# Optimization experiments

Hardware: AMD Instinct MI355X
Metric: run time of the kernel (lower is better)

## Reference

```python
import jax, jax.numpy as jnp
import numpy as np

L, H, DH = 4, 8, 64            # num_layers, num_heads, hidden_dim (= dim_per_head)
HD = H * DH                    # 512 = per-layer q/k/v width
R, BLOCK, NREG, NW = 3, 128, 8, 8   # n_hashes, block_size, num_regions, num_w_per_dist
CDIM, LAT = 2, 3               # coords_dim, latent_dim
SCALE = 1.0 / float(np.sqrt(DH))


def layer_norm(x, g, b):
    m = x.mean(-1, keepdims=True)
    v = ((x - m) ** 2).mean(-1, keepdims=True)
    return (x - m) * jax.lax.rsqrt(v + 1e-5) * g + b


def hept_attention(q, k, v, coords, batch, w_head, hash_proj):
    # HEPT: E2LSH hash + region/batch bucketing -> sort -> blockwise attention
    # with RPE distance bias, combined over hash rounds by logsumexp weights.
    N = q.shape[0]
    nb = N // BLOCK
    qh = q.reshape(N, H, DH)
    kh = k.reshape(N, H, DH)
    vh = v.reshape(N, H, DH)
    c0 = coords[:, 0]
    region = jnp.clip(((c0 - c0.min()) / (c0.max() - c0.min() + 1e-6) * NREG).astype(jnp.int32), 0, NREG - 1)
    c_rpe = coords[:, 1:]                       # [N, CDIM-1] dims used for RPE distances
    bf = batch.astype(jnp.float32)
    outs, lses = [], []
    for r in range(R):
        hv = coords @ hash_proj[r]              # [N] LSH projection
        hn = (hv - hv.min()) / (hv.max() - hv.min() + 1e-6)
        skey = (bf * NREG + region.astype(jnp.float32)) * 2.0 + hn  # batch-major, region, hash
        idx = jnp.argsort(skey)
        inv = jnp.argsort(idx)
        qs = qh[idx].reshape(nb, BLOCK, H, DH)
        ks = kh[idx].reshape(nb, BLOCK, H, DH)
        vs = vh[idx].reshape(nb, BLOCK, H, DH)
        cs = c_rpe[idx].reshape(nb, BLOCK, CDIM - 1)
        bs = batch[idx].reshape(nb, BLOCK)
        scores = jnp.einsum('bihd,bjhd->bhij', qs, ks) * SCALE     # [nb,H,B,B]
        d2 = (cs[:, :, None, :] - cs[:, None, :, :]) ** 2          # [nb,B,B,CDIM-1]
        scores = scores - jnp.einsum('hc,bijc->bhij', w_head, d2)  # RPE distance penalty
        scores = jnp.where((bs[:, :, None] == bs[:, None, :])[:, None], scores, -1e9)
        lse = jax.nn.logsumexp(scores, axis=-1)                    # [nb,H,B]
        p = jnp.exp(scores - lse[..., None])
        o = jnp.einsum('bhij,bjhd->bihd', p, vs).reshape(N, H, DH)
        outs.append(o[inv])
        lses.append(jnp.transpose(lse, (0, 2, 1)).reshape(N, H)[inv])
    wts = jax.nn.softmax(jnp.stack(lses), axis=0)[..., None]       # [R,N,H,1]
    return (wts * jnp.stack(outs)).sum(0).reshape(N, HD)


def _forward(x, coords, batch, enc_W1, enc_b1, enc_W2, enc_b2, ln1_g, ln1_b, wq, wk, wv,
             rpe_W, wo, ln2_g, ln2_b, ff_W1, ff_b1, ff_W2, ff_b2, W_cat,
             mlp_W1, mlp_b1, mlp_W2, mlp_b2, beta_W1, beta_b1, beta_W2, beta_b2,
             coord_W1, coord_b1, coord_W2, coord_b2, hash_proj):
    h0 = jax.nn.relu(x @ enc_W1 + enc_b1) @ enc_W2 + enc_b2
    feats = [h0]
    cur = h0
    for l in range(L):
        xn = layer_norm(cur, ln1_g[l], ln1_b[l])
        q = xn @ wq[l]
        k = xn @ wk[l]
        v = xn @ wv[l]
        # per-head positive RPE weights derived from w_rpe weight matrix
        w_head = jax.nn.softplus(rpe_W[l].reshape(CDIM - 1, NW, H, DH).mean(axis=(1, 3)).T)  # [H,CDIM-1]
        a = hept_attention(q, k, v, coords, batch, w_head, hash_proj) @ wo[l]
        cur = cur + a
        ffo = jax.nn.relu(layer_norm(cur, ln2_g[l], ln2_b[l]) @ ff_W1[l] + ff_b1[l]) @ ff_W2[l] + ff_b2[l]
        cur = cur + ffo
        feats.append(cur)
    enc2 = jnp.concatenate(feats, axis=-1) @ W_cat
    out = enc2 + (jax.nn.relu(enc2 @ mlp_W1 + mlp_b1) @ mlp_W2 + mlp_b2)
    eps = 1e-6
    beta = jnp.clip(jax.nn.sigmoid(jax.nn.relu(out @ beta_W1 + beta_b1) @ beta_W2 + beta_b2), eps, 1.0 - eps)
    hcoord = jax.nn.relu(out @ coord_W1 + coord_b1) @ coord_W2 + coord_b2
    return beta, hcoord


def setup_inputs() -> dict:
    key = jax.random.key(0)
    ks = jax.random.split(key, 40)
    N, IN_DIM = 32768, 16
    def w(i, shape, s=0.05):
        return jax.random.normal(ks[i], shape, jnp.float32) * s
    return dict(
        x=jax.random.normal(ks[0], (N, IN_DIM), jnp.float32),
        coords=jax.random.normal(ks[1], (N, CDIM), jnp.float32),
        batch=jnp.sort(jax.random.randint(ks[2], (N,), 0, 8)),
        enc_W1=w(3, (IN_DIM, DH)), enc_b1=jnp.zeros((DH,), jnp.float32),
        enc_W2=w(4, (DH, DH)), enc_b2=jnp.zeros((DH,), jnp.float32),
        ln1_g=jnp.ones((L, DH), jnp.float32), ln1_b=jnp.zeros((L, DH), jnp.float32),
        wq=w(5, (L, DH, HD)), wk=w(6, (L, DH, HD)), wv=w(7, (L, DH, HD)),
        rpe_W=w(8, (L, NW * (CDIM - 1), HD)),
        wo=w(9, (L, HD, DH)),
        ln2_g=jnp.ones((L, DH), jnp.float32), ln2_b=jnp.zeros((L, DH), jnp.float32),
        ff_W1=w(10, (L, DH, DH)), ff_b1=jnp.zeros((L, DH), jnp.float32),
        ff_W2=w(11, (L, DH, DH)), ff_b2=jnp.zeros((L, DH), jnp.float32),
        W_cat=w(12, (DH * (L + 1), DH // 2)),
        mlp_W1=w(13, (DH // 2, DH // 2)), mlp_b1=jnp.zeros((DH // 2,), jnp.float32),
        mlp_W2=w(14, (DH // 2, DH // 2)), mlp_b2=jnp.zeros((DH // 2,), jnp.float32),
        beta_W1=w(15, (DH // 2, DH // 4)), beta_b1=jnp.zeros((DH // 4,), jnp.float32),
        beta_W2=w(16, (DH // 4, 1)), beta_b2=jnp.zeros((1,), jnp.float32),
        coord_W1=w(17, (DH // 2, DH // 4)), coord_b1=jnp.zeros((DH // 4,), jnp.float32),
        coord_W2=w(18, (DH // 4, LAT)), coord_b2=jnp.zeros((LAT,), jnp.float32),
        hash_proj=jax.random.normal(ks[19], (R, CDIM), jnp.float32),
    )


def reference(x, coords, batch, enc_W1, enc_b1, enc_W2, enc_b2, ln1_g, ln1_b, wq, wk, wv,
              rpe_W, wo, ln2_g, ln2_b, ff_W1, ff_b1, ff_W2, ff_b2, W_cat,
              mlp_W1, mlp_b1, mlp_W2, mlp_b2, beta_W1, beta_b1, beta_W2, beta_b2,
              coord_W1, coord_b1, coord_W2, coord_b2, hash_proj):
    return _forward(x, coords, batch, enc_W1, enc_b1, enc_W2, enc_b2, ln1_g, ln1_b, wq, wk, wv,
                    rpe_W, wo, ln2_g, ln2_b, ff_W1, ff_b1, ff_W2, ff_b2, W_cat,
                    mlp_W1, mlp_b1, mlp_W2, mlp_b2, beta_W1, beta_b1, beta_W2, beta_b2,
                    coord_W1, coord_b1, coord_W2, coord_b2, hash_proj)
```

## Files before the change

### kernel.cpp

```cpp
#include <hip/hip_runtime.h>
#include <math.h>

#define DEV __device__ __forceinline__

constexpr int DHc = 64;
constexpr int HDc = 512;
constexpr int Hc  = 8;
constexpr int BLKc = 128;

typedef float f32x16 __attribute__((ext_vector_type(16)));
typedef short s16x8  __attribute__((ext_vector_type(8)));

union FragU { unsigned u[4]; s16x8 v; };

DEV unsigned fenc(float f){ unsigned u = __float_as_uint(f); return (u & 0x80000000u) ? ~u : (u | 0x80000000u); }
DEV float fdec(unsigned u){ unsigned b = (u & 0x80000000u) ? (u ^ 0x80000000u) : ~u; return __uint_as_float(b); }
DEV float hv_calc(float c0, float c1, float h0, float h1){
  return __fadd_rn(__fmul_rn(c0, h0), __fmul_rn(c1, h1));
}
DEV unsigned short f2bf(float f){
  unsigned u = __float_as_uint(f);
  return (unsigned short)((u + 0x7FFFu + ((u >> 16) & 1u)) >> 16);
}
DEV float bf2f(unsigned short s){ return __uint_as_float((unsigned)s << 16); }

DEV unsigned cvtpk(float lo, float hi){
  unsigned r;
  asm("v_cvt_pk_bf16_f32 %0, %1, %2" : "=v"(r) : "v"(lo), "v"(hi));
  return r;
}
DEV unsigned pack_bf2(float lo, float hi){
  return (unsigned)f2bf(lo) | ((unsigned)f2bf(hi) << 16);
}
DEV void pswap(unsigned &a, unsigned &b){
  asm volatile("v_permlane32_swap_b32 %0, %1" : "+v"(a), "+v"(b));
}

__global__ void minmax_init_kernel(unsigned* mm){
  int t = threadIdx.x;
  if (t < 4) mm[t] = 0xFFFFFFFFu;
  else if (t < 8) mm[t] = 0u;
}

__global__ __launch_bounds__(256) void minmax_reduce_kernel(const float* __restrict__ coords,
    const float* __restrict__ hp, unsigned* mm, int N)
{
  __shared__ float red[4][8];
  float h[6];
  #pragma unroll
  for (int i = 0; i < 6; ++i) h[i] = hp[i];
  float mn[4] = {3.0e38f, 3.0e38f, 3.0e38f, 3.0e38f};
  float mx[4] = {-3.0e38f, -3.0e38f, -3.0e38f, -3.0e38f};
  for (int i = blockIdx.x*blockDim.x + threadIdx.x; i < N; i += gridDim.x*blockDim.x){
    float2 c = *(const float2*)&coords[2*i];
    float v0 = c.x;
    float v1 = hv_calc(c.x, c.y, h[0], h[1]);
    float v2 = hv_calc(c.x, c.y, h[2], h[3]);
    float v3 = hv_calc(c.x, c.y, h[4], h[5]);
    mn[0] = fminf(mn[0], v0); mx[0] = fmaxf(mx[0], v0);
    mn[1] = fminf(mn[1], v1); mx[1] = fmaxf(mx[1], v1);
    mn[2] = fminf(mn[2], v2); mx[2] = fmaxf(mx[2], v2);
    mn[3] = fminf(mn[3], v3); mx[3] = fmaxf(mx[3], v3);
  }
  #pragma unroll
  for (int o = 1; o < 64; o <<= 1){
    #pragma unroll
    for (int s = 0; s < 4; ++s){
      mn[s] = fminf(mn[s], __shfl_xor(mn[s], o));
      mx[s] = fmaxf(mx[s], __shfl_xor(mx[s], o));
    }
  }
  int w = threadIdx.x >> 6;
  if ((threadIdx.x & 63) == 0){
    #pragma unroll
    for (int s = 0; s < 4; ++s){ red[w][s] = mn[s]; red[w][4+s] = mx[s]; }
  }
  __syncthreads();
  int t = threadIdx.x;
  if (t < 4){
    float v = fminf(fminf(red[0][t], red[1][t]), fminf(red[2][t], red[3][t]));
    atomicMin(&mm[t], fenc(v));
  } else if (t < 8){
    float v = fmaxf(fmaxf(red[0][t], red[1][t]), fmaxf(red[2][t], red[3][t]));
    atomicMax(&mm[t], fenc(v));
  }
}

__global__ void make_keys_kernel(const float* __restrict__ coords, const int* __restrict__ batch,
                                 const float* __restrict__ hp, const unsigned* __restrict__ mm,
                                 unsigned long long* __restrict__ keys, int N)
{
  int i = blockIdx.x*blockDim.x + threadIdx.x;
  if (i >= N) return;
  float c0 = coords[2*i], c1 = coords[2*i+1];
  float c0min = fdec(mm[0]), c0max = fdec(mm[4]);
  float rf = (c0 - c0min) / (c0max - c0min + 1e-6f) * 8.0f;
  int region = (int)rf;
  region = region < 0 ? 0 : (region > 7 ? 7 : region);
  float base2 = ((float)batch[i] * 8.0f + (float)region) * 2.0f;
  #pragma unroll
  for (int r = 0; r < 3; ++r){
    float hv = hv_calc(c0, c1, hp[2*r], hp[2*r+1]);
    float hn = (hv - fdec(mm[1+r])) / (fdec(mm[5+r]) - fdec(mm[1+r]) + 1e-6f);
    float skey = base2 + hn;
    keys[(size_t)r*N + i] = ((unsigned long long)__float_as_uint(skey) << 32) | (unsigned)i;
  }
}

__global__ __launch_bounds__(1024) void bitonic_local_full2k_kernel(unsigned long long* keys, int N)
{
  __shared__ unsigned long long sh[2048];
  unsigned long long* a = keys + (size_t)blockIdx.y * N;
  int base = blockIdx.x * 2048, t = threadIdx.x;
  sh[t] = a[base + t];
  sh[t + 1024] = a[base + t + 1024];
  __syncthreads();
  for (int k = 2; k <= 2048; k <<= 1){
    for (int j = k >> 1; j > 0; j >>= 1){
      int i = ((t & ~(j-1)) << 1) | (t & (j-1));
      bool dirup = (((base + i) & k) == 0);
      unsigned long long x = sh[i], y = sh[i+j];
      if ((x > y) == dirup){ sh[i] = y; sh[i+j] = x; }
      __syncthreads();
    }
  }
  a[base + t] = sh[t];
  a[base + t + 1024] = sh[t + 1024];
}

__global__ void bitonic_global_kernel(unsigned long long* keys, int N, int k, int j)
{
  unsigned long long* a = keys + (size_t)blockIdx.y * N;
  int i = blockIdx.x*blockDim.x + threadIdx.x;
  int l = i ^ j;
  if (l > i && l < N){
    unsigned long long x = a[i], y = a[l];
    bool dirup = ((i & k) == 0);
    if ((x > y) == dirup){ a[i] = y; a[l] = x; }
  }
}

__global__ __launch_bounds__(1024) void bitonic_local_merge2k_kernel(unsigned long long* keys, int N, int k)
{
  __shared__ unsigned long long sh[2048];
  unsigned long long* a = keys + (size_t)blockIdx.y * N;
  int base = blockIdx.x * 2048, t = threadIdx.x;
  sh[t] = a[base + t];
  sh[t + 1024] = a[base + t + 1024];
  __syncthreads();
  for (int j = 1024; j > 0; j >>= 1){
    int i = ((t & ~(j-1)) << 1) | (t & (j-1));
    bool dirup = (((base + i) & k) == 0);
    unsigned long long x = sh[i], y = sh[i+j];
    if ((x > y) == dirup){ sh[i] = y; sh[i+j] = x; }
    __syncthreads();
  }
  a[base + t] = sh[t];
  a[base + t + 1024] = sh[t + 1024];
}

__global__ void extract_idx_kernel(const unsigned long long* __restrict__ keys, int* __restrict__ idx, int total)
{
  int i = blockIdx.x*blockDim.x + threadIdx.x;
  if (i < total) idx[i] = (int)(keys[i] & 0xFFFFFFFFull);
}

__global__ void wconv_kernel(const float* __restrict__ wq, const float* __restrict__ wk,
                             const float* __restrict__ wv, const float* __restrict__ wo,
                             unsigned short* __restrict__ wqkvT, unsigned short* __restrict__ woT)
{
  int tid = blockIdx.x*blockDim.x + threadIdx.x;
  const int NQ = 4*3*512*64;
  if (tid < NQ){
    int kk = tid & 63;
    int rest = tid >> 6;
    int n = rest & 511;
    int rest2 = rest >> 9;
    int z = rest2 % 3, l = rest2 / 3;
    const float* W = (z==0) ? wq : (z==1) ? wk : wv;
    wqkvT[tid] = f2bf(W[((size_t)l*64 + kk)*512 + n]);
  } else if (tid < NQ + 4*64*512){
    int e = tid - NQ;
    int kk = e & 511;
    int rest = e >> 9;
    int n = rest & 63;
    int l = rest >> 6;
    woT[e] = f2bf(wo[((size_t)l*512 + kk)*64 + n]);
  }
}

__global__ __launch_bounds__(256) void mqk_kernel(const float* __restrict__ wq,
    const float* __restrict__ wk, unsigned short* __restrict__ mqk)
{
  __shared__ float qs[64][64];
  __shared__ float ks_[64][64];
  int blk = blockIdx.x;
  int l = blk >> 3, h = blk & 7;
  int t = threadIdx.x;
  for (int f = t; f < 4096; f += 256){
    int i = f >> 6, d = f & 63;
    qs[i][d]  = wq[((size_t)l*64 + i)*512 + h*64 + d];
    ks_[i][d] = wk[((size_t)l*64 + i)*512 + h*64 + d];
  }
  __syncthreads();
  int j = t >> 2, i0 = (t & 3) * 16;
  unsigned short* outp = mqk + (size_t)blk*4096 + j*64;
  #pragma unroll
  for (int ii = 0; ii < 16; ++ii){
    int i = i0 + ii;
    float acc = 0.f;
    #pragma unroll
    for (int d = 0; d < 64; ++d) acc += qs[i][d]*ks_[j][d];
    outp[i] = f2bf(acc * 0.125f);
  }
}

__global__ __launch_bounds__(256) void encoder_kernel(const float* __restrict__ x,
    const float* __restrict__ W1, const float* __restrict__ b1,
    const float* __restrict__ W2, const float* __restrict__ b2,
    const float* __restrict__ lng, const float* __restrict__ lnb,
    float* __restrict__ h0, unsigned short* __restrict__ xnb, int N)
{
  __shared__ float W1s[16][64];
  __shared__ __align__(16) float W2s[64][64];
  __shared__ float xs[4][16];
  __shared__ float t1s[4][64];
  int t = threadIdx.x;
  for (int f = t; f < 1024; f += 256) W1s[f>>6][f&63] = W1[f];
  #pragma unroll
  for (int e = 0; e < 4; ++e){ int f = t + e*256; *(float4*)&W2s[f>>4][(f&15)*4] = *(const float4*)&W2[f*4]; }
  int w = t >> 6, d = t & 63;
  int row = blockIdx.x*4 + w;
  if (d < 16) xs[w][d] = x[(size_t)row*16 + d];
  __syncthreads();
  float acc = b1[d];
  #pragma unroll
  for (int i = 0; i < 16; ++i) acc += xs[w][i]*W1s[i][d];
  t1s[w][d] = fmaxf(acc, 0.f);
  __syncthreads();
  float acc2 = b2[d];
  #pragma unroll
  for (int i = 0; i < 64; ++i) acc2 += t1s[w][i]*W2s[i][d];
  h0[(size_t)row*64 + d] = acc2;
  float s = acc2;
  #pragma unroll
  for (int o = 1; o < 64; o <<= 1) s += __shfl_xor(s, o);
  float mean = s * (1.0f/64.0f);
  float dv = acc2 - mean, sq = dv*dv;
  #pragma unroll
  for (int o = 1; o < 64; o <<= 1) sq += __shfl_xor(sq, o);
  xnb[(size_t)row*64 + d] = f2bf(dv * rsqrtf(sq*(1.0f/64.0f) + 1e-5f) * lng[d] + lnb[d]);
}

__global__ void whead_kernel(const float* __restrict__ rpe, float* __restrict__ wh)
{
  int l = blockIdx.x >> 3, h = blockIdx.x & 7, d = threadIdx.x;
  const float* rp = rpe + (size_t)l*8*512;
  float s = 0.f;
  #pragma unroll
  for (int w = 0; w < 8; ++w) s += rp[(size_t)w*512 + h*64 + d];
  #pragma unroll
  for (int o = 1; o < 64; o <<= 1) s += __shfl_xor(s, o);
  if (d == 0){
    float m = s * (1.0f/512.0f);
    wh[blockIdx.x] = fmaxf(m, 0.f) + log1pf(expf(-fabsf(m)));
  }
}

__global__ __launch_bounds__(256, 3) void attn_kernel(
    const unsigned short* __restrict__ xnb, const unsigned short* __restrict__ wqkvT_l,
    const unsigned short* __restrict__ mqk_l,
    const float* __restrict__ coords, const int* __restrict__ batch,
    const int* __restrict__ idx_all, const float* __restrict__ w_head,
    float* __restrict__ lse_all, unsigned short* __restrict__ o_buf, int N)
{
  __shared__ __align__(16) unsigned short xlds[128*64];
  __shared__ __align__(16) unsigned short tlds[128*64];
  __shared__ __align__(16) unsigned short vtl[64*128];
  __shared__ __align__(16) float c1s[BLKc];
  __shared__ __align__(16) int   bts[BLKc];
  __shared__ int   idxs[BLKc];
  __shared__ __align__(16) float isel[BLKc];
  __shared__ int unif;
  int b = blockIdx.x, h = blockIdx.y, r = blockIdx.z, t = threadIdx.x;
  const int* idx_r = idx_all + (size_t)r*N;
  if (t < BLKc){
    int g = idx_r[b*BLKc + t];
    idxs[t] = g; c1s[t] = coords[2*g+1]; bts[t] = batch[g];
  }
  __syncthreads();
  if (t == 0) unif = (bts[0] == bts[127]);
  #pragma unroll
  for (int e = 0; e < 4; ++e){
    int f = t + e*256;
    int row = f >> 3, ch = f & 7;
    int g = idxs[row];
    s16x8 xv = *(const s16x8*)&xnb[(size_t)g*64 + ch*8];
    *(s16x8*)&xlds[row*64 + ((ch ^ (row&7))*8)] = xv;
  }
  __syncthreads();

  int w = t >> 6, l = t & 63, lo = l & 31, hi = l >> 5;
  int arow = w*32 + lo;

  s16x8 af[4];
  #pragma unroll
  for (int ks = 0; ks < 4; ++ks)
    af[ks] = *(const s16x8*)&xlds[arow*64 + ((((ks<<1)|hi) ^ (arow&7))*8)];

  {
    const unsigned short* Mt = mqk_l + (size_t)h*4096;
    f32x16 a0, a1;
    #pragma unroll
    for (int i = 0; i < 16; ++i){ a0[i] = 0.f; a1[i] = 0.f; }
    #pragma unroll
    for (int ks = 0; ks < 4; ++ks){
      s16x8 b0 = *(const s16x8*)&Mt[(size_t)(lo)*64      + ks*16 + hi*8];
      s16x8 b1 = *(const s16x8*)&Mt[(size_t)(32 + lo)*64 + ks*16 + hi*8];
      a0 = __builtin_amdgcn_mfma_f32_32x32x16_bf16(af[ks], b0, a0, 0, 0, 0);
      a1 = __builtin_amdgcn_mfma_f32_32x32x16_bf16(af[ks], b1, a1, 0, 0, 0);
    }
    int ch0 = lo >> 3, ch1 = 4 + (lo >> 3), co = lo & 7;
    #pragma unroll
    for (int reg = 0; reg < 16; ++reg){
      int row = w*32 + (reg&3) + 8*(reg>>2) + 4*hi;
      tlds[row*64 + ((ch0 ^ (row&7))*8) + co] = f2bf(a0[reg]);
      tlds[row*64 + ((ch1 ^ (row&7))*8) + co] = f2bf(a1[reg]);
    }
  }
  {
    const unsigned short* wz = wqkvT_l + (size_t)2*512*64 + (size_t)h*64*64;
    f32x16 a0, a1;
    #pragma unroll
    for (int i = 0; i < 16; ++i){ a0[i] = 0.f; a1[i] = 0.f; }
    #pragma unroll
    for (int ks = 0; ks < 4; ++ks){
      s16x8 b0 = *(const s16x8*)&wz[(size_t)(lo)*64      + ks*16 + hi*8];
      s16x8 b1 = *(const s16x8*)&wz[(size_t)(32 + lo)*64 + ks*16 + hi*8];
      a0 = __builtin_amdgcn_mfma_f32_32x32x16_bf16(af[ks], b0, a0, 0, 0, 0);
      a1 = __builtin_amdgcn_mfma_f32_32x32x16_bf16(af[ks], b1, a1, 0, 0, 0);
    }
    #pragma unroll
    for (int rq = 0; rq < 4; ++rq){
      int k0 = w*32 + rq*8 + 4*hi;
      int cj = k0 >> 3;
      int d0 = lo, d1 = 32 + lo;
      unsigned* dp0 = (unsigned*)&vtl[d0*128 + ((cj ^ (d0&7))*8) + 4*hi];
      dp0[0] = pack_bf2(a0[rq*4+0], a0[rq*4+1]);
      dp0[1] = pack_bf2(a0[rq*4+2], a0[rq*4+3]);
      unsigned* dp1 = (unsigned*)&vtl[d1*128 + ((cj ^ (d1&7))*8) + 4*hi];
      dp1[0] = pack_bf2(a1[rq*4+0], a1[rq*4+1]);
      dp1[1] = pack_bf2(a1[rq*4+2], a1[rq*4+3]);
    }
  }
  __syncthreads();

  int qrow = arow;
  s16x8 tf[4];
  #pragma unroll
  for (int ks = 0; ks < 4; ++ks)
    tf[ks] = *(const s16x8*)&tlds[qrow*64 + ((((ks<<1)|hi) ^ (qrow&7))*8)];

  f32x16 acc[4];
  #pragma unroll
  for (int kt = 0; kt < 4; ++kt)
    #pragma unroll
    for (int i = 0; i < 16; ++i) acc[kt][i] = 0.f;

  __builtin_amdgcn_s_setprio(1);
  #pragma unroll
  for (int kt = 0; kt < 4; ++kt){
    int krow = kt*32 + lo;
    #pragma unroll
    for (int ks = 0; ks < 4; ++ks){
      s16x8 xf = *(const s16x8*)&xlds[krow*64 + ((((ks<<1)|hi) ^ (krow&7))*8)];
      acc[kt] = __builtin_amdgcn_mfma_f32_32x32x16_bf16(xf, tf[ks], acc[kt], 0, 0, 0);
    }
  }
  __builtin_amdgcn_s_setprio(0);

  float c1i = c1s[qrow]; int bti = bts[qrow];
  float wh = w_head[h];
  float se = 0.f;
#define SCORE_LOOP(MASKED)                                                   \
  _Pragma("unroll")                                                          \
  for (int kt = 0; kt < 4; ++kt){                                            \
    _Pragma("unroll")                                                        \
    for (int rq = 0; rq < 4; ++rq){                                          \
      int kb = kt*32 + rq*8 + hi*4;                                          \
      float4 c4 = *(const float4*)&c1s[kb];                                  \
      int4  b4 = *(const int4*)&bts[kb];                                     \
      _Pragma("unroll")                                                      \
      for (int j = 0; j < 4; ++j){                                           \
        int reg = rq*4 + j;                                                  \
        float c1k = (j==0)?c4.x:(j==1)?c4.y:(j==2)?c4.z:c4.w;                \
        int   btk = (j==0)?b4.x:(j==1)?b4.y:(j==2)?b4.z:b4.w;                \
        float dd = c1i - c1k;                                                \
        float sc = acc[kt][reg] - wh*dd*dd;                                  \
        if (MASKED && bti != btk) sc = -1e9f;                                \
        float pv = __expf(sc);                                               \
        acc[kt][reg] = pv;                                                   \
        se += pv;                                                            \
      }                                                                      \
    }                                                                        \
  }
  if (unif){ SCORE_LOOP(false) } else { SCORE_LOOP(true) }
#undef SCORE_LOOP
  se += __shfl_xor(se, 32);
  if (l < 32){
    int gi0 = idxs[qrow];
    lse_all[((size_t)r*N + gi0)*Hc + h] = __logf(se);
    isel[qrow] = 1.0f / se;
  }

  f32x16 oa0, oa1;
  #pragma unroll
  for (int i = 0; i < 16; ++i){ oa0[i] = 0.f; oa1[i] = 0.f; }

  __builtin_amdgcn_s_setprio(1);
  #pragma unroll
  for (int kt = 0; kt < 4; ++kt){
    unsigned X = cvtpk(acc[kt][0],  acc[kt][1]);
    unsigned Z = cvtpk(acc[kt][2],  acc[kt][3]);
    unsigned Y = cvtpk(acc[kt][4],  acc[kt][5]);
    unsigned W = cvtpk(acc[kt][6],  acc[kt][7]);
    pswap(X, Y); pswap(Z, W);
    FragU f0; f0.u[0]=X; f0.u[1]=Z; f0.u[2]=Y; f0.u[3]=W;
    unsigned X2 = cvtpk(acc[kt][8],  acc[kt][9]);
    unsigned Z2 = cvtpk(acc[kt][10], acc[kt][11]);
    unsigned Y2 = cvtpk(acc[kt][12], acc[kt][13]);
    unsigned W2 = cvtpk(acc[kt][14], acc[kt][15]);
    pswap(X2, Y2); pswap(Z2, W2);
    FragU f1; f1.u[0]=X2; f1.u[1]=Z2; f1.u[2]=Y2; f1.u[3]=W2;
    #pragma unroll
    for (int hks = 0; hks < 2; ++hks){
      s16x8 pa = hks ? f1.v : f0.v;
      int kch = kt*4 + hks*2 + hi;
      int d0 = lo;
      s16x8 vf0 = *(const s16x8*)&vtl[d0*128 + ((kch ^ (d0&7))*8)];
      oa0 = __builtin_amdgcn_mfma_f32_32x32x16_bf16(pa, vf0, oa0, 0, 0, 0);
      int d1 = 32 + lo;
      s16x8 vf1 = *(const s16x8*)&vtl[d1*128 + ((kch ^ (d1&7))*8)];
      oa1 = __builtin_amdgcn_mfma_f32_32x32x16_bf16(pa, vf1, oa1, 0, 0, 0);
    }
  }
  __builtin_amdgcn_s_setprio(0);

  unsigned short* orow = o_buf + (size_t)r*N*HDc;
  #pragma unroll
  for (int rq = 0; rq < 4; ++rq){
    float4 s4 = *(const float4*)&isel[w*32 + rq*8 + hi*4];
    #pragma unroll
    for (int j = 0; j < 4; ++j){
      int reg = rq*4 + j;
      int qq = rq*8 + hi*4 + j;
      int g = idxs[w*32 + qq];
      float sv = (j==0)?s4.x:(j==1)?s4.y:(j==2)?s4.z:s4.w;
      unsigned short* dst = &orow[(size_t)g*HDc + h*DHc + lo];
      dst[0]  = f2bf(oa0[reg]*sv);
      dst[32] = f2bf(oa1[reg]*sv);
    }
  }
  (void)b;
}

__global__ __launch_bounds__(256) void wo_mfma_kernel(
    const unsigned short* __restrict__ o_buf, const float* __restrict__ lse_all,
    const unsigned short* __restrict__ woT_l, float* __restrict__ cur, int N)
{
  __shared__ __align__(16) unsigned short As[64*128];
  __shared__ __align__(16) unsigned short Bs[64*128];
  __shared__ float wts[64][24];
  int rb = blockIdx.x*64, t = threadIdx.x;
  #pragma unroll
  for (int e = 0; e < 2; ++e){
    int p = t + e*256;
    int rr = p >> 3, h = p & 7;
    float l0 = lse_all[((size_t)0*N + rb+rr)*Hc + h];
    float l1 = lse_all[((size_t)1*N + rb+rr)*Hc + h];
    float l2 = lse_all[((size_t)2*N + rb+rr)*Hc + h];
    float lm = fmaxf(l0, fmaxf(l1, l2));
    float e0 = __expf(l0-lm), e1 = __expf(l1-lm), e2 = __expf(l2-lm);
    float inv = 1.0f/(e0+e1+e2);
    wts[rr][h*3+0] = e0*inv; wts[rr][h*3+1] = e1*inv; wts[rr][h*3+2] = e2*inv;
  }
  int w = t >> 6, l = t & 63, lo = l & 31, hi = l >> 5;
  int mt = w >> 1, nt = w & 1;
  f32x16 acc;
  #pragma unroll
  for (int i = 0; i < 16; ++i) acc[i] = 0.f;
  for (int kt = 0; kt < 4; ++kt){
    __syncthreads();
    #pragma unroll
    for (int e = 0; e < 4; ++e){
      int f = t + e*256; int rr = f >> 4, kc = f & 15;
      int k0 = kt*128 + kc*8;
      int h = k0 >> 6;
      float w0 = wts[rr][h*3+0], w1 = wts[rr][h*3+1], w2 = wts[rr][h*3+2];
      s16x8 u0 = *(const s16x8*)&o_buf[((size_t)0*N + rb+rr)*HDc + k0];
      s16x8 u1 = *(const s16x8*)&o_buf[((size_t)1*N + rb+rr)*HDc + k0];
      s16x8 u2 = *(const s16x8*)&o_buf[((size_t)2*N + rb+rr)*HDc + k0];
      FragU fo;
      #pragma unroll
      for (int ii = 0; ii < 4; ++ii){
        float a0 = w0*bf2f((unsigned short)u0[2*ii])   + w1*bf2f((unsigned short)u1[2*ii])   + w2*bf2f((unsigned short)u2[2*ii]);
        float a1 = w0*bf2f((unsigned short)u0[2*ii+1]) + w1*bf2f((unsigned short)u1[2*ii+1]) + w2*bf2f((unsigned short)u2[2*ii+1]);
        fo.u[ii] = cvtpk(a0, a1);
      }
      *(s16x8*)&As[rr*128 + ((kc ^ (rr&7))*8)] = fo.v;
      *(s16x8*)&Bs[rr*128 + ((kc ^ (rr&7))*8)] = *(const s16x8*)&woT_l[(size_t)rr*512 + k0];
    }
    __syncthreads();
    #pragma unroll
    for (int ks = 0; ks < 8; ++ks){
      int s = ks*2 + hi;
      int arow = mt*32 + lo, brow = nt*32 + lo;
      s16x8 af = *(const s16x8*)&As[arow*128 + ((s ^ (arow&7))*8)];
      s16x8 bfr = *(const s16x8*)&Bs[brow*128 + ((s ^ (brow&7))*8)];
      acc = __builtin_amdgcn_mfma_f32_32x32x16_bf16(af, bfr, acc, 0, 0, 0);
    }
  }
  #pragma unroll
  for (int reg = 0; reg < 16; ++reg){
    int m = mt*32 + (reg&3) + 8*(reg>>2) + 4*hi;
    int n = nt*32 + lo;
    cur[(size_t)(rb+m)*64 + n] += acc[reg];
  }
}

__global__ __launch_bounds__(256) void ffn_kernel(float* __restrict__ cur,
    const float* __restrict__ g, const float* __restrict__ bln,
    const float* __restrict__ W1, const float* __restrict__ b1,
    const float* __restrict__ W2, const float* __restrict__ b2,
    const float* __restrict__ nlg, const float* __restrict__ nlb,
    unsigned short* __restrict__ xnb, int N)
{
  __shared__ __align__(16) float W1s[64][64];
  __shared__ __align__(16) float W2s[64][64];
  __shared__ float xns[4][64];
  __shared__ float t1s[4][64];
  int t = threadIdx.x;
  #pragma unroll
  for (int e = 0; e < 4; ++e){
    int f = t + e*256; int rr = f >> 4, c4 = f & 15;
    *(float4*)&W1s[rr][c4*4] = *(const float4*)&W1[f*4];
    *(float4*)&W2s[rr][c4*4] = *(const float4*)&W2[f*4];
  }
  int w = t >> 6, d = t & 63;
  int row = blockIdx.x*4 + w;
  float v = cur[(size_t)row*64 + d];
  float s = v;
  #pragma unroll
  for (int o = 1; o < 64; o <<= 1) s += __shfl_xor(s, o);
  float mean = s * (1.0f/64.0f);
  float dv = v - mean, sq = dv*dv;
  #pragma unroll
  for (int o = 1; o < 64; o <<= 1) sq += __shfl_xor(sq, o);
  float xnv = dv * rsqrtf(sq*(1.0f/64.0f) + 1e-5f) * g[d] + bln[d];
  xns[w][d] = xnv;
  __syncthreads();
  float acc = b1[d];
  #pragma unroll
  for (int i = 0; i < 64; ++i) acc += xns[w][i]*W1s[i][d];
  t1s[w][d] = fmaxf(acc, 0.f);
  __syncthreads();
  float acc2 = b2[d];
  #pragma unroll
  for (int i = 0; i < 64; ++i) acc2 += t1s[w][i]*W2s[i][d];
  float nv = v + acc2;
  cur[(size_t)row*64 + d] = nv;
  if (nlg){
    float s2 = nv;
    #pragma unroll
    for (int o = 1; o < 64; o <<= 1) s2 += __shfl_xor(s2, o);
    float mean2 = s2 * (1.0f/64.0f);
    float dv2 = nv - mean2, sq2 = dv2*dv2;
    #pragma unroll
    for (int o = 1; o < 64; o <<= 1) sq2 += __shfl_xor(sq2, o);
    xnb[(size_t)row*64 + d] = f2bf(dv2 * rsqrtf(sq2*(1.0f/64.0f) + 1e-5f) * nlg[d] + nlb[d]);
  }
}

__global__ __launch_bounds__(256) void enc2_accum_kernel(const float* __restrict__ cur,
    const float* __restrict__ Wcat, float* __restrict__ enc2, int rowoff, int store, int N)
{
  __shared__ float Ws[64][33];
  __shared__ float crs[32][65];
  int t = threadIdx.x;
  for (int f = t; f < 2048; f += 256) Ws[f>>5][f&31] = Wcat[(size_t)(rowoff + (f>>5))*32 + (f&31)];
  for (int f = t; f < 2048; f += 256) crs[f>>6][f&63] = cur[(size_t)(blockIdx.x*32 + (f>>6))*64 + (f&63)];
  __syncthreads();
  int r8 = t >> 5, c = t & 31;
  for (int rr = r8; rr < 32; rr += 8){
    int row = blockIdx.x*32 + rr;
    float acc = 0.f;
    #pragma unroll
    for (int d = 0; d < 64; ++d) acc += crs[rr][d]*Ws[d][c];
    size_t o = (size_t)row*32 + c;
    if (store) enc2[o] = acc; else enc2[o] += acc;
  }
}

__global__ __launch_bounds__(256) void head_kernel(const float* __restrict__ enc2,
    const float* mW1, const float* mb1, const float* mW2, const float* mb2,
    const float* bW1, const float* bb1, const float* bW2, const float* bb2,
    const float* cW1, const float* cb1, const float* cW2, const float* cb2,
    float* __restrict__ outp, int N)
{
  __shared__ float s_mW1[32][32], s_mW2[32][32], s_bW1[32][16], s_cW1[32][16];
  __shared__ float s_bW2[16], s_cW2[16][3];
  __shared__ float e2[8][32], t1[8][32], ov[8][32], bt[8][16], ct[8][16];
  int t = threadIdx.x;
  for (int f = t; f < 1024; f += 256){ s_mW1[f>>5][f&31] = mW1[f]; s_mW2[f>>5][f&31] = mW2[f]; }
  for (int f = t; f < 512; f += 256){ s_bW1[f>>4][f&15] = bW1[f]; s_cW1[f>>4][f&15] = cW1[f]; }
  if (t < 16) s_bW2[t] = bW2[t];
  if (t < 48) s_cW2[t/3][t%3] = cW2[t];
  int r8 = t >> 5, c = t & 31;
  int row = blockIdx.x*8 + r8;
  float e = enc2[(size_t)row*32 + c];
  e2[r8][c] = e;
  __syncthreads();
  float a = mb1[c];
  #pragma unroll
  for (int i = 0; i < 32; ++i) a += e2[r8][i]*s_mW1[i][c];
  t1[r8][c] = fmaxf(a, 0.f);
  __syncthreads();
  float o = e + mb2[c];
  #pragma unroll
  for (int i = 0; i < 32; ++i) o += t1[r8][i]*s_mW2[i][c];
  ov[r8][c] = o;
  __syncthreads();
  if (c < 16){
    float a2 = bb1[c];
    #pragma unroll
    for (int i = 0; i < 32; ++i) a2 += ov[r8][i]*s_bW1[i][c];
    bt[r8][c] = fmaxf(a2, 0.f);
  } else {
    int cc = c - 16;
    float a2 = cb1[cc];
    #pragma unroll
    for (int i = 0; i < 32; ++i) a2 += ov[r8][i]*s_cW1[i][cc];
    ct[r8][cc] = fmaxf(a2, 0.f);
  }
  __syncthreads();
  if (c == 0){
    float a3 = bb2[0];
    #pragma unroll
    for (int i = 0; i < 16; ++i) a3 += bt[r8][i]*s_bW2[i];
    float sg = 1.0f / (1.0f + __expf(-a3));
    sg = fminf(fmaxf(sg, 1e-6f), 1.0f - 1e-6f);
    outp[row] = sg;
  } else if (c < 4){
    int dd = c - 1;
    float a3 = cb2[dd];
    #pragma unroll
    for (int i = 0; i < 16; ++i) a3 += ct[r8][i]*s_cW2[i][dd];
    outp[(size_t)N + (size_t)row*3 + dd] = a3;
  }
}

extern "C" void kernel_launch(void* const* d_in, const int* in_sizes, int n_in,
                              void* d_out, int out_size, void* d_ws, size_t ws_size,
                              hipStream_t stream)
{
  const float* x       = (const float*)d_in[0];
  const float* coords  = (const float*)d_in[1];
  const int*   batch   = (const int*)d_in[2];
  const float* enc_W1  = (const float*)d_in[3];
  const float* enc_b1  = (const float*)d_in[4];
  const float* enc_W2  = (const float*)d_in[5];
  const float* enc_b2  = (const float*)d_in[6];
  const float* ln1_g   = (const float*)d_in[7];
  const float* ln1_b   = (const float*)d_in[8];
  const float* wq      = (const float*)d_in[9];
  const float* wk      = (const float*)d_in[10];
  const float* wv      = (const float*)d_in[11];
  const float* rpe_W   = (const float*)d_in[12];
  const float* wo      = (const float*)d_in[13];
  const float* ln2_g   = (const float*)d_in[14];
  const float* ln2_b   = (const float*)d_in[15];
  const float* ff_W1   = (const float*)d_in[16];
  const float* ff_b1   = (const float*)d_in[17];
  const float* ff_W2   = (const float*)d_in[18];
  const float* ff_b2   = (const float*)d_in[19];
  const float* W_cat   = (const float*)d_in[20];
  const float* mlp_W1  = (const float*)d_in[21];
  const float* mlp_b1  = (const float*)d_in[22];
  const float* mlp_W2  = (const float*)d_in[23];
  const float* mlp_b2  = (const float*)d_in[24];
  const float* beta_W1 = (const float*)d_in[25];
  const float* beta_b1 = (const float*)d_in[26];
  const float* beta_W2 = (const float*)d_in[27];
  const float* beta_b2 = (const float*)d_in[28];
  const float* coord_W1= (const float*)d_in[29];
  const float* coord_b1= (const float*)d_in[30];
  const float* coord_W2= (const float*)d_in[31];
  const float* coord_b2= (const float*)d_in[32];
  const float* hash_proj=(const float*)d_in[33];

  const int N  = in_sizes[0] / 16;
  const int nb = N / 128;
  float* outp = (float*)d_out;
  (void)out_size; (void)ws_size; (void)n_in;

  char* p = (char*)d_ws;
  size_t off = 0;
  auto alloc = [&](size_t bytes) -> char* {
    char* r = p + off;
    off += (bytes + 255) & ~(size_t)255;
    return r;
  };
  float* cur    = (float*)alloc((size_t)N*64*4);
  unsigned short* xnb = (unsigned short*)alloc((size_t)N*64*2);
  unsigned short* o_buf = (unsigned short*)alloc((size_t)3*N*512*2);
  float* enc2   = (float*)alloc((size_t)N*32*4);
  float* lse    = (float*)alloc((size_t)3*N*8*4);
  unsigned long long* keys = (unsigned long long*)alloc((size_t)3*N*8);
  int* idx      = (int*)alloc((size_t)3*N*4);
  unsigned short* wqkvT = (unsigned short*)alloc((size_t)4*3*512*64*2);
  unsigned short* woT   = (unsigned short*)alloc((size_t)4*64*512*2);
  unsigned short* mqk   = (unsigned short*)alloc((size_t)4*8*64*64*2);
  unsigned* mm  = (unsigned*)alloc(256);
  float* whead  = (float*)alloc(256);

  wconv_kernel<<<2048, 256, 0, stream>>>(wq, wk, wv, wo, wqkvT, woT);
  mqk_kernel<<<32, 256, 0, stream>>>(wq, wk, mqk);
  whead_kernel<<<32, 64, 0, stream>>>(rpe_W, whead);

  minmax_init_kernel<<<1, 64, 0, stream>>>(mm);
  minmax_reduce_kernel<<<64, 256, 0, stream>>>(coords, hash_proj, mm, N);
  make_keys_kernel<<<(N+255)/256, 256, 0, stream>>>(coords, batch, hash_proj, mm, keys, N);
  bitonic_local_full2k_kernel<<<dim3(N/2048, 3), 1024, 0, stream>>>(keys, N);
  for (int kk = 4096; kk <= N; kk <<= 1){
    for (int j = kk >> 1; j >= 2048; j >>= 1)
      bitonic_global_kernel<<<dim3(N/256, 3), 256, 0, stream>>>(keys, N, kk, j);
    bitonic_local_merge2k_kernel<<<dim3(N/2048, 3), 1024, 0, stream>>>(keys, N, kk);
  }
  extract_idx_kernel<<<(3*N+255)/256, 256, 0, stream>>>(keys, idx, 3*N);

  encoder_kernel<<<N/4, 256, 0, stream>>>(x, enc_W1, enc_b1, enc_W2, enc_b2,
      ln1_g, ln1_b, cur, xnb, N);
  enc2_accum_kernel<<<N/32, 256, 0, stream>>>(cur, W_cat, enc2, 0, 1, N);

  for (int l = 0; l < 4; ++l){
    attn_kernel<<<dim3(nb, 8, 3), 256, 0, stream>>>(xnb,
        wqkvT + (size_t)l*3*512*64, mqk + (size_t)l*8*4096,
        coords, batch, idx, whead + l*8, lse, o_buf, N);
    wo_mfma_kernel<<<N/64, 256, 0, stream>>>(o_buf, lse, woT + (size_t)l*64*512, cur, N);
    const float* nlg = (l < 3) ? (ln1_g + (l+1)*64) : nullptr;
    const float* nlb = (l < 3) ? (ln1_b + (l+1)*64) : nullptr;
    ffn_kernel<<<N/4, 256, 0, stream>>>(cur, ln2_g + l*64, ln2_b + l*64,
        ff_W1 + (size_t)l*64*64, ff_b1 + l*64, ff_W2 + (size_t)l*64*64, ff_b2 + l*64,
        nlg, nlb, xnb, N);
    enc2_accum_kernel<<<N/32, 256, 0, stream>>>(cur, W_cat, enc2, (l+1)*64, 0, N);
  }

  head_kernel<<<N/8, 256, 0, stream>>>(enc2, mlp_W1, mlp_b1, mlp_W2, mlp_b2,
      beta_W1, beta_b1, beta_W2, beta_b2, coord_W1, coord_b1, coord_W2, coord_b2, outp, N);
}
```

Measured before the change: 727.0 us.

## Keep Q·M fragments in registers and fold softmax normalization into hash-combine

The transformed query tile is computed with swapped MFMA operands and repacked into B-fragments in registers via permlane swaps, so the tlds shared buffer and one barrier go away. The attention kernel now writes raw exp-sums and unnormalized outputs, and the output projection kernel combines the three hash rounds as a sum divided by the total exp-sum, dropping the log/exp weighting. This cuts LDS use, which allows raising the launch-bounds occupancy hint to 4. The risks are unnormalized bf16 outputs losing precision, exp-sums that can overflow because there is no max subtraction, and register pressure under the tighter occupancy bound.

```diff
diff --git a/kernel.cpp b/kernel.cpp
--- a/kernel.cpp
+++ b/kernel.cpp
@@ -34,6 +34,16 @@
 }
 DEV void pswap(unsigned &a, unsigned &b){
   asm volatile("v_permlane32_swap_b32 %0, %1" : "+v"(a), "+v"(b));
+}
+DEV s16x8 pack_frag(const f32x16 &s, int half){
+  int b = half*8;
+  unsigned X = pack_bf2(s[b+0], s[b+1]);
+  unsigned Z = pack_bf2(s[b+2], s[b+3]);
+  unsigned Y = pack_bf2(s[b+4], s[b+5]);
+  unsigned W = pack_bf2(s[b+6], s[b+7]);
+  pswap(X, Y); pswap(Z, W);
+  FragU f; f.u[0]=X; f.u[1]=Z; f.u[2]=Y; f.u[3]=W;
+  return f.v;
 }
 
 __global__ void minmax_init_kernel(unsigned* mm){
@@ -267,20 +277,18 @@
   }
 }
 
-__global__ __launch_bounds__(256, 3) void attn_kernel(
+__global__ __launch_bounds__(256, 4) void attn_kernel(
     const unsigned short* __restrict__ xnb, const unsigned short* __restrict__ wqkvT_l,
     const unsigned short* __restrict__ mqk_l,
     const float* __restrict__ coords, const int* __restrict__ batch,
     const int* __restrict__ idx_all, const float* __restrict__ w_head,
-    float* __restrict__ lse_all, unsigned short* __restrict__ o_buf, int N)
+    float* __restrict__ se_all, unsigned short* __restrict__ o_buf, int N)
 {
   __shared__ __align__(16) unsigned short xlds[128*64];
-  __shared__ __align__(16) unsigned short tlds[128*64];
   __shared__ __align__(16) unsigned short vtl[64*128];
   __shared__ __align__(16) float c1s[BLKc];
   __shared__ __align__(16) int   bts[BLKc];
   __shared__ int   idxs[BLKc];
-  __shared__ __align__(16) float isel[BLKc];
   __shared__ int unif;
   int b = blockIdx.x, h = blockIdx.y, r = blockIdx.z, t = threadIdx.x;
   const int* idx_r = idx_all + (size_t)r*N;
@@ -308,25 +316,23 @@
   for (int ks = 0; ks < 4; ++ks)
     af[ks] = *(const s16x8*)&xlds[arow*64 + ((((ks<<1)|hi) ^ (arow&7))*8)];
 
+  s16x8 tf[4];
   {
     const unsigned short* Mt = mqk_l + (size_t)h*4096;
-    f32x16 a0, a1;
-    #pragma unroll
-    for (int i = 0; i < 16; ++i){ a0[i] = 0.f; a1[i] = 0.f; }
+    f32x16 t0, t1;
+    #pragma unroll
+    for (int i = 0; i < 16; ++i){ t0[i] = 0.f; t1[i] = 0.f; }
     #pragma unroll
     for (int ks = 0; ks < 4; ++ks){
-      s16x8 b0 = *(const s16x8*)&Mt[(size_t)(lo)*64      + ks*16 + hi*8];
-      s16x8 b1 = *(const s16x8*)&Mt[(size_t)(32 + lo)*64 + ks*16 + hi*8];
-      a0 = __builtin_amdgcn_mfma_f32_32x32x16_bf16(af[ks], b0, a0, 0, 0, 0);
-      a1 = __builtin_amdgcn_mfma_f32_32x32x16_bf16(af[ks], b1, a1, 0, 0, 0);
-    }
-    int ch0 = lo >> 3, ch1 = 4 + (lo >> 3), co = lo & 7;
-    #pragma unroll
-    for (int reg = 0; reg < 16; ++reg){
-      int row = w*32 + (reg&3) + 8*(reg>>2) + 4*hi;
-      tlds[row*64 + ((ch0 ^ (row&7))*8) + co] = f2bf(a0[reg]);
-      tlds[row*64 + ((ch1 ^ (row&7))*8) + co] = f2bf(a1[reg]);
-    }
+      s16x8 m0 = *(const s16x8*)&Mt[(size_t)(lo)*64      + ks*16 + hi*8];
+      s16x8 m1 = *(const s16x8*)&Mt[(size_t)(32 + lo)*64 + ks*16 + hi*8];
+      t0 = __builtin_amdgcn_mfma_f32_32x32x16_bf16(m0, af[ks], t0, 0, 0, 0);
+      t1 = __builtin_amdgcn_mfma_f32_32x32x16_bf16(m1, af[ks], t1, 0, 0, 0);
+    }
+    tf[0] = pack_frag(t0, 0);
+    tf[1] = pack_frag(t0, 1);
+    tf[2] = pack_frag(t1, 0);
+    tf[3] = pack_frag(t1, 1);
   }
   {
     const unsigned short* wz = wqkvT_l + (size_t)2*512*64 + (size_t)h*64*64;
@@ -353,14 +359,8 @@
       dp1[1] = pack_bf2(a1[rq*4+2], a1[rq*4+3]);
     }
   }
-  __syncthreads();
 
   int qrow = arow;
-  s16x8 tf[4];
-  #pragma unroll
-  for (int ks = 0; ks < 4; ++ks)
-    tf[ks] = *(const s16x8*)&tlds[qrow*64 + ((((ks<<1)|hi) ^ (qrow&7))*8)];
-
   f32x16 acc[4];
   #pragma unroll
   for (int kt = 0; kt < 4; ++kt)
@@ -409,9 +409,9 @@
   se += __shfl_xor(se, 32);
   if (l < 32){
     int gi0 = idxs[qrow];
-    lse_all[((size_t)r*N + gi0)*Hc + h] = __logf(se);
-    isel[qrow] = 1.0f / se;
-  }
+    se_all[((size_t)r*N + gi0)*Hc + h] = se;
+  }
+  __syncthreads();
 
   f32x16 oa0, oa1;
   #pragma unroll
@@ -449,40 +449,35 @@
   unsigned short* orow = o_buf + (size_t)r*N*HDc;
   #pragma unroll
   for (int rq = 0; rq < 4; ++rq){
-    float4 s4 = *(const float4*)&isel[w*32 + rq*8 + hi*4];
     #pragma unroll
     for (int j = 0; j < 4; ++j){
       int reg = rq*4 + j;
       int qq = rq*8 + hi*4 + j;
       int g = idxs[w*32 + qq];
-      float sv = (j==0)?s4.x:(j==1)?s4.y:(j==2)?s4.z:s4.w;
       unsigned short* dst = &orow[(size_t)g*HDc + h*DHc + lo];
-      dst[0]  = f2bf(oa0[reg]*sv);
-      dst[32] = f2bf(oa1[reg]*sv);
+      dst[0]  = f2bf(oa0[reg]);
+      dst[32] = f2bf(oa1[reg]);
     }
   }
   (void)b;
 }
 
 __global__ __launch_bounds__(256) void wo_mfma_kernel(
-    const unsigned short* __restrict__ o_buf, const float* __restrict__ lse_all,
+    const unsigned short* __restrict__ o_buf, const float* __restrict__ se_all,
     const unsigned short* __restrict__ woT_l, float* __restrict__ cur, int N)
 {
   __shared__ __align__(16) unsigned short As[64*128];
   __shared__ __align__(16) unsigned short Bs[64*128];
-  __shared__ float wts[64][24];
+  __shared__ float invs[64][9];
   int rb = blockIdx.x*64, t = threadIdx.x;
   #pragma unroll
   for (int e = 0; e < 2; ++e){
     int p = t + e*256;
     int rr = p >> 3, h = p & 7;
-    float l0 = lse_all[((size_t)0*N + rb+rr)*Hc + h];
-    float l1 = lse_all[((size_t)1*N + rb+rr)*Hc + h];
-    float l2 = lse_all[((size_t)2*N + rb+rr)*Hc + h];
-    float lm = fmaxf(l0, fmaxf(l1, l2));
-    float e0 = __expf(l0-lm), e1 = __expf(l1-lm), e2 = __expf(l2-lm);
-    float inv = 1.0f/(e0+e1+e2);
-    wts[rr][h*3+0] = e0*inv; wts[rr][h*3+1] = e1*inv; wts[rr][h*3+2] = e2*inv;
+    float s0 = se_all[((size_t)0*N + rb+rr)*Hc + h];
+    float s1 = se_all[((size_t)1*N + rb+rr)*Hc + h];
+    float s2 = se_all[((size_t)2*N + rb+rr)*Hc + h];
+    invs[rr][h] = 1.0f/(s0+s1+s2);
   }
   int w = t >> 6, l = t & 63, lo = l & 31, hi = l >> 5;
   int mt = w >> 1, nt = w & 1;
@@ -496,15 +491,15 @@
       int f = t + e*256; int rr = f >> 4, kc = f & 15;
       int k0 = kt*128 + kc*8;
       int h = k0 >> 6;
-      float w0 = wts[rr][h*3+0], w1 = wts[rr][h*3+1], w2 = wts[rr][h*3+2];
+      float inv = invs[rr][h];
       s16x8 u0 = *(const s16x8*)&o_buf[((size_t)0*N + rb+rr)*HDc + k0];
       s16x8 u1 = *(const s16x8*)&o_buf[((size_t)1*N + rb+rr)*HDc + k0];
       s16x8 u2 = *(const s16x8*)&o_buf[((size_t)2*N + rb+rr)*HDc + k0];
       FragU fo;
       #pragma unroll
       for (int ii = 0; ii < 4; ++ii){
-        float a0 = w0*bf2f((unsigned short)u0[2*ii])   + w1*bf2f((unsigned short)u1[2*ii])   + w2*bf2f((unsigned short)u2[2*ii]);
-        float a1 = w0*bf2f((unsigned short)u0[2*ii+1]) + w1*bf2f((unsigned short)u1[2*ii+1]) + w2*bf2f((unsigned short)u2[2*ii+1]);
+        float a0 = (bf2f((unsigned short)u0[2*ii])   + bf2f((unsigned short)u1[2*ii])   + bf2f((unsigned short)u2[2*ii]))   * inv;
+        float a1 = (bf2f((unsigned short)u0[2*ii+1]) + bf2f((unsigned short)u1[2*ii+1]) + bf2f((unsigned short)u2[2*ii+1])) * inv;
         fo.u[ii] = cvtpk(a0, a1);
       }
       *(s16x8*)&As[rr*128 + ((kc ^ (rr&7))*8)] = fo.v;
@@ -714,7 +709,7 @@
   unsigned short* xnb = (unsigned short*)alloc((size_t)N*64*2);
   unsigned short* o_buf = (unsigned short*)alloc((size_t)3*N*512*2);
   float* enc2   = (float*)alloc((size_t)N*32*4);
-  float* lse    = (float*)alloc((size_t)3*N*8*4);
+  float* se_buf = (float*)alloc((size_t)3*N*8*4);
   unsigned long long* keys = (unsigned long long*)alloc((size_t)3*N*8);
   int* idx      = (int*)alloc((size_t)3*N*4);
   unsigned short* wqkvT = (unsigned short*)alloc((size_t)4*3*512*64*2);
@@ -745,8 +740,8 @@
   for (int l = 0; l < 4; ++l){
     attn_kernel<<<dim3(nb, 8, 3), 256, 0, stream>>>(xnb,
         wqkvT + (size_t)l*3*512*64, mqk + (size_t)l*8*4096,
-        coords, batch, idx, whead + l*8, lse, o_buf, N);
-    wo_mfma_kernel<<<N/64, 256, 0, stream>>>(o_buf, lse, woT + (size_t)l*64*512, cur, N);
+        coords, batch, idx, whead + l*8, se_buf, o_buf, N);
+    wo_mfma_kernel<<<N/64, 256, 0, stream>>>(o_buf, se_buf, woT + (size_t)l*64*512, cur, N);
     const float* nlg = (l < 3) ? (ln1_g + (l+1)*64) : nullptr;
     const float* nlb = (l < 3) ? (ln1_b + (l+1)*64) : nullptr;
     ffn_kernel<<<N/4, 256, 0, stream>>>(cur, ln2_g + l*64, ln2_b + l*64,
```

New measurement: 974.1 us. 34.0% more time.
